# Kernel optimization log

Hardware: AMD Instinct MI355X
Metric: run time of the kernel (lower is better)

The kernel has to match this reference:

```python
import jax, jax.numpy as jnp
import numpy as np

B, T, C, L = 256, 256, 1024, 32
NEG = -1e30   # log-domain 'zero'
EPS = 1e-7    # keras.backend.epsilon()


def setup_inputs() -> dict:
    key = jax.random.key(0)
    k1, k2 = jax.random.split(key)
    # ctc_batch_cost expects softmax probabilities
    y_pred = jax.nn.softmax(jax.random.normal(k1, (B, T, C), dtype=jnp.float32), axis=-1)
    # labels in [1, C-2]: 0 is padding (count_nonzero), C-1 is the CTC blank
    y_true = jax.random.randint(k2, (B, L), 1, C - 1).astype(jnp.int32)
    return {"y_true": y_true, "y_pred": y_pred}


def _ctc_batch_cost(y_true, y_pred):
    b, t, c = y_pred.shape
    blank = c - 1                                   # TF ctc_loss: blank = last class
    lp = jnp.log(y_pred + EPS)                      # [B,T,C]
    l = y_true.shape[1]
    s = 2 * l + 1                                   # extended label length
    labels = y_true.astype(jnp.int32)
    # extended label seq: blank, l1, blank, l2, ..., blank
    ext = jnp.full((b, s), blank, jnp.int32).at[:, 1::2].set(labels)  # [B,S]
    label_len = jnp.sum((y_true != 0).astype(jnp.int32), axis=1)      # [B]
    # gather per-step log-probs of extended labels -> [B,T,S]
    lp_ext = jnp.take_along_axis(lp, jnp.broadcast_to(ext[:, None, :], (b, t, s)), axis=2)
    # skip transition s-2 -> s allowed iff ext[s] != blank and ext[s] != ext[s-2]
    prev2 = jnp.concatenate([jnp.full((b, 2), -1, jnp.int32), ext[:, :-2]], axis=1)
    allow_skip = (ext != blank) & (ext != prev2)    # [B,S]

    alpha = jnp.full((b, s), NEG, lp.dtype)
    alpha = alpha.at[:, 0].set(lp_ext[:, 0, 0]).at[:, 1].set(lp_ext[:, 0, 1])
    lp_t = jnp.transpose(lp_ext, (1, 0, 2))         # [T,B,S]

    def step(a, lpt):
        a1 = a
        a2 = jnp.concatenate([jnp.full((b, 1), NEG, a.dtype), a[:, :-1]], axis=1)
        a3 = jnp.concatenate([jnp.full((b, 2), NEG, a.dtype), a[:, :-2]], axis=1)
        a3 = jnp.where(allow_skip, a3, NEG)
        a_new = lpt + jnp.logaddexp(jnp.logaddexp(a1, a2), a3)
        return a_new, None

    alpha, _ = jax.lax.scan(step, alpha, lp_t[1:])  # input_length == T (full)
    bi = jnp.arange(b)
    idx_last_blank = 2 * label_len                  # position 2*Lb (last blank)
    idx_last_label = 2 * label_len - 1
    loss = -jnp.logaddexp(alpha[bi, idx_last_blank], alpha[bi, idx_last_label])
    return loss[:, None]                            # [B,1], matches ctc_batch_cost


def reference(y_true, y_pred):
    return _ctc_batch_cost(y_true, y_pred)
```

## Files before the change

kernel.cpp:

```cpp
#include <hip/hip_runtime.h>
#include <math.h>


#define Bt 256
#define Tt 256
#define Ct 1024
#define Lt 32
#define NEGV (-1e30f)
#define EPSV (1e-7f)
#define WAVES 16
#define TPW (Tt / WAVES)
#define STRIDE 33

__device__ __forceinline__ float lae2(float a, float b) {
    float m = fmaxf(a, b);
    return m + __logf(__expf(a - m) + __expf(b - m));
}
__device__ __forceinline__ float lae3(float a, float b, float c) {
    float m = fmaxf(fmaxf(a, b), c);
    return m + __logf(__expf(a - m) + __expf(b - m) + __expf(c - m));
}

__global__ __launch_bounds__(1024) void ctc_kernel(const int* __restrict__ y_true,
                                                   const float* __restrict__ y_pred,
                                                   float* __restrict__ out) {
    __shared__ float s_lp[Tt * STRIDE];
    __shared__ float s_alpha[66];

    const int b = blockIdx.x;
    const int tid = threadIdx.x;
    const int w = tid >> 6;
    const int lane = tid & 63;
    const int blank = Ct - 1;
    const float* yp = y_pred + (size_t)b * Tt * Ct;
    const int* lab = y_true + b * Lt;

    int cls = blank;
    if (lane < 32) cls = lab[lane];

    if (lane < 33) {
        const int t0 = w * TPW;
        float v[TPW];
        #pragma unroll
        for (int k = 0; k < TPW; ++k)
            v[k] = yp[(size_t)(t0 + k) * Ct + cls];
        #pragma unroll
        for (int k = 0; k < TPW; ++k)
            s_lp[(t0 + k) * STRIDE + lane] = __logf(v[k] + EPSV);
    }
    __syncthreads();

    if (w == 0) {
        bool allow = true;
        if (lane >= 1 && lane < 32) {
            int lprev = lab[lane - 1];
            allow = (cls != blank) && (cls != lprev);
        }

        unsigned long long nz = __ballot(lane < 32 && cls != 0);
        int ll = (int)__popcll(nz);

        float a_even, a_odd;
        {
            float le = s_lp[32];
            float lo = (lane < 32) ? s_lp[lane] : NEGV;
            a_even = (lane == 0) ? le : NEGV;
            a_odd  = (lane == 0) ? lo : NEGV;
        }

        #pragma unroll 4
        for (int t = 1; t < Tt; ++t) {
            float le = s_lp[t * STRIDE + 32];
            float lo = (lane < 32) ? s_lp[t * STRIDE + lane] : NEGV;
            float po = __shfl_up(a_odd, 1);
            if (lane == 0) po = NEGV;
            float ne = le + lae2(a_even, po);
            float no = lo + lae3(a_odd, a_even, allow ? po : NEGV);
            a_even = ne;
            a_odd  = no;
        }

        if (lane < 33) {
            s_alpha[2 * lane] = a_even;
            if (lane < 32) s_alpha[2 * lane + 1] = a_odd;
        }
        __builtin_amdgcn_s_waitcnt(0);
        if (lane == 0) {
            int i1 = 2 * ll;
            int i2 = 2 * ll - 1;
            float v1 = s_alpha[i1];
            float v2 = (i2 >= 0) ? s_alpha[i2] : NEGV;
            out[b] = -lae2(v1, v2);
        }
    }
}

extern "C" void kernel_launch(void* const* d_in, const int* in_sizes, int n_in,
                              void* d_out, int out_size, void* d_ws, size_t ws_size,
                              hipStream_t stream) {
    const int* y_true = (const int*)d_in[0];
    const float* y_pred = (const float*)d_in[1];
    float* out = (float*)d_out;
    (void)in_sizes; (void)n_in; (void)out_size; (void)d_ws; (void)ws_size;
    ctc_kernel<<<Bt, 1024, 0, stream>>>(y_true, y_pred, out);
}
```

Measured before the change: 375.4 us.

## Stream full rows via coalesced float4 loads into LDS staging before gather

Replaces scattered per-lane gathers of 33 label probabilities per time step with fully coalesced float4 reads of whole 8-row chunks of y_pred into a shared staging buffer, double-buffered through registers, then gathers from LDS. The aim is to avoid uncoalesced, latency-bound global accesses. In exchange the kernel reads the entire 1 MB per batch row instead of only the needed elements, which is about 30x more global traffic, and it adds 64 block-wide barriers.

```diff
diff --git a/kernel.cpp b/kernel.cpp
--- a/kernel.cpp
+++ b/kernel.cpp
@@ -8,9 +8,10 @@
 #define Lt 32
 #define NEGV (-1e30f)
 #define EPSV (1e-7f)
-#define WAVES 16
-#define TPW (Tt / WAVES)
-#define STRIDE 33
+#define SLP 34
+#define RPC 8
+#define NC (Tt / RPC)
+#define F4PC (RPC * Ct / 4)
 
 __device__ __forceinline__ float lae2(float a, float b) {
     float m = fmaxf(a, b);
@@ -24,7 +25,8 @@
 __global__ __launch_bounds__(1024) void ctc_kernel(const int* __restrict__ y_true,
                                                    const float* __restrict__ y_pred,
                                                    float* __restrict__ out) {
-    __shared__ float s_lp[Tt * STRIDE];
+    __shared__ float s_lp[Tt * SLP];
+    __shared__ float s_stage[RPC * Ct];
     __shared__ float s_alpha[66];
 
     const int b = blockIdx.x;
@@ -32,23 +34,40 @@
     const int w = tid >> 6;
     const int lane = tid & 63;
     const int blank = Ct - 1;
-    const float* yp = y_pred + (size_t)b * Tt * Ct;
+    const float4* yp4 = (const float4*)(y_pred + (size_t)b * Tt * Ct);
     const int* lab = y_true + b * Lt;
 
     int cls = blank;
     if (lane < 32) cls = lab[lane];
 
-    if (lane < 33) {
-        const int t0 = w * TPW;
-        float v[TPW];
-        #pragma unroll
-        for (int k = 0; k < TPW; ++k)
-            v[k] = yp[(size_t)(t0 + k) * Ct + cls];
-        #pragma unroll
-        for (int k = 0; k < TPW; ++k)
-            s_lp[(t0 + k) * STRIDE + lane] = __logf(v[k] + EPSV);
+    float4* s_stage4 = (float4*)s_stage;
+
+    {
+        float4 r0 = yp4[tid];
+        float4 r1 = yp4[tid + 1024];
+        s_stage4[tid] = r0;
+        s_stage4[tid + 1024] = r1;
     }
     __syncthreads();
+
+    for (int c = 0; c < NC; ++c) {
+        float4 r0, r1;
+        const bool more = (c + 1 < NC);
+        if (more) {
+            r0 = yp4[(c + 1) * F4PC + tid];
+            r1 = yp4[(c + 1) * F4PC + tid + 1024];
+        }
+        if (w < RPC && lane < 33) {
+            int t = c * RPC + w;
+            s_lp[t * SLP + lane] = __logf(s_stage[w * Ct + cls] + EPSV);
+        }
+        __syncthreads();
+        if (more) {
+            s_stage4[tid] = r0;
+            s_stage4[tid + 1024] = r1;
+            __syncthreads();
+        }
+    }
 
     if (w == 0) {
         bool allow = true;
@@ -56,7 +75,6 @@
             int lprev = lab[lane - 1];
             allow = (cls != blank) && (cls != lprev);
         }
-
         unsigned long long nz = __ballot(lane < 32 && cls != 0);
         int ll = (int)__popcll(nz);
 
@@ -70,8 +88,8 @@
 
         #pragma unroll 4
         for (int t = 1; t < Tt; ++t) {
-            float le = s_lp[t * STRIDE + 32];
-            float lo = (lane < 32) ? s_lp[t * STRIDE + lane] : NEGV;
+            float le = s_lp[t * SLP + 32];
+            float lo = (lane < 32) ? s_lp[t * SLP + lane] : NEGV;
             float po = __shfl_up(a_odd, 1);
             if (lane == 0) po = NEGV;
             float ne = le + lae2(a_even, po);
```

Measured after the change: 393.1 us. 4.7% more time.

## Split CTC into parallel gather kernel and single-wave recurrence kernel

Applied to the files above, without the earlier changes.

The fused per-batch kernel, with 1024 threads and a large shared buffer, is replaced by two kernels. A fully parallel gather kernel writes the log-probs of the extended labels to a workspace. A 64-thread-per-batch recurrence kernel then streams those values from global memory with a 16-deep register prefetch and uses shuffles in place of shared memory for the blank value and the final readout. The aim is to stop 15 idle waves and a large LDS allocation from limiting occupancy during the serial recurrence, and to overlap the loads with computation. In exchange it adds a workspace round trip and a second launch. The prefetch also reads past the end of each batch's rows, into the next batch's region and beyond the workspace for the last batch.

```diff
diff --git a/kernel.cpp b/kernel.cpp
--- a/kernel.cpp
+++ b/kernel.cpp
@@ -6,11 +6,10 @@
 #define Tt 256
 #define Ct 1024
 #define Lt 32
+#define NSEL 33
+#define TOTE (Bt * Tt * NSEL)
 #define NEGV (-1e30f)
 #define EPSV (1e-7f)
-#define WAVES 16
-#define TPW (Tt / WAVES)
-#define STRIDE 33
 
 __device__ __forceinline__ float lae2(float a, float b) {
     float m = fmaxf(a, b);
@@ -21,78 +20,66 @@
     return m + __logf(__expf(a - m) + __expf(b - m) + __expf(c - m));
 }
 
-__global__ __launch_bounds__(1024) void ctc_kernel(const int* __restrict__ y_true,
-                                                   const float* __restrict__ y_pred,
-                                                   float* __restrict__ out) {
-    __shared__ float s_lp[Tt * STRIDE];
-    __shared__ float s_alpha[66];
+__global__ __launch_bounds__(256) void ctc_gather(const int* __restrict__ y_true,
+                                                  const float* __restrict__ y_pred,
+                                                  float* __restrict__ ws) {
+    unsigned e = blockIdx.x * 256u + threadIdx.x;
+    unsigned row = e / 33u;
+    unsigned j = e - row * 33u;
+    unsigned b = row >> 8;
+    int cls = Ct - 1;
+    if (j < 32u) cls = y_true[(b << 5) + j];
+    float v = y_pred[((size_t)row << 10) + (unsigned)cls];
+    ws[e] = __logf(v + EPSV);
+}
 
+__global__ __launch_bounds__(64) void ctc_rec(const int* __restrict__ y_true,
+                                              const float* __restrict__ ws,
+                                              float* __restrict__ out) {
     const int b = blockIdx.x;
-    const int tid = threadIdx.x;
-    const int w = tid >> 6;
-    const int lane = tid & 63;
-    const int blank = Ct - 1;
-    const float* yp = y_pred + (size_t)b * Tt * Ct;
+    const int lane = threadIdx.x;
+    const int li = (lane < 33) ? lane : 32;
+    const float* lp = ws + (size_t)b * Tt * NSEL;
     const int* lab = y_true + b * Lt;
 
-    int cls = blank;
-    if (lane < 32) cls = lab[lane];
+    int cls = (lane < 32) ? lab[lane] : (Ct - 1);
+    bool allow = true;
+    if (lane >= 1 && lane < 32) {
+        int lprev = lab[lane - 1];
+        allow = (cls != Ct - 1) && (cls != lprev);
+    }
+    unsigned long long nz = __ballot(lane < 32 && cls != 0);
+    int ll = (int)__popcll(nz);
 
-    if (lane < 33) {
-        const int t0 = w * TPW;
-        float v[TPW];
+    float buf[16];
+    #pragma unroll
+    for (int k = 0; k < 16; ++k) buf[k] = lp[k * NSEL + li];
+
+    float a_even = NEGV, a_odd = NEGV;
+    for (int g = 0; g < 16; ++g) {
         #pragma unroll
-        for (int k = 0; k < TPW; ++k)
-            v[k] = yp[(size_t)(t0 + k) * Ct + cls];
-        #pragma unroll
-        for (int k = 0; k < TPW; ++k)
-            s_lp[(t0 + k) * STRIDE + lane] = __logf(v[k] + EPSV);
-    }
-    __syncthreads();
-
-    if (w == 0) {
-        bool allow = true;
-        if (lane >= 1 && lane < 32) {
-            int lprev = lab[lane - 1];
-            allow = (cls != blank) && (cls != lprev);
-        }
-
-        unsigned long long nz = __ballot(lane < 32 && cls != 0);
-        int ll = (int)__popcll(nz);
-
-        float a_even, a_odd;
-        {
-            float le = s_lp[32];
-            float lo = (lane < 32) ? s_lp[lane] : NEGV;
-            a_even = (lane == 0) ? le : NEGV;
-            a_odd  = (lane == 0) ? lo : NEGV;
-        }
-
-        #pragma unroll 4
-        for (int t = 1; t < Tt; ++t) {
-            float le = s_lp[t * STRIDE + 32];
-            float lo = (lane < 32) ? s_lp[t * STRIDE + lane] : NEGV;
-            float po = __shfl_up(a_odd, 1);
-            if (lane == 0) po = NEGV;
-            float ne = le + lae2(a_even, po);
-            float no = lo + lae3(a_odd, a_even, allow ? po : NEGV);
-            a_even = ne;
-            a_odd  = no;
-        }
-
-        if (lane < 33) {
-            s_alpha[2 * lane] = a_even;
-            if (lane < 32) s_alpha[2 * lane + 1] = a_odd;
-        }
-        __builtin_amdgcn_s_waitcnt(0);
-        if (lane == 0) {
-            int i1 = 2 * ll;
-            int i2 = 2 * ll - 1;
-            float v1 = s_alpha[i1];
-            float v2 = (i2 >= 0) ? s_alpha[i2] : NEGV;
-            out[b] = -lae2(v1, v2);
+        for (int k = 0; k < 16; ++k) {
+            float cur = buf[k];
+            buf[k] = lp[((unsigned)((g + 1) * 16 + k)) * NSEL + li];
+            float le = __shfl(cur, 32);
+            float lo = (lane < 32) ? cur : NEGV;
+            if (k == 0 && g == 0) {
+                a_even = (lane == 0) ? le : NEGV;
+                a_odd  = (lane == 0) ? lo : NEGV;
+            } else {
+                float po = __shfl_up(a_odd, 1);
+                if (lane == 0) po = NEGV;
+                float ne = le + lae2(a_even, po);
+                float no = lo + lae3(a_odd, a_even, allow ? po : NEGV);
+                a_even = ne;
+                a_odd  = no;
+            }
         }
     }
+
+    float v1 = __shfl(a_even, ll);
+    float v2 = (ll >= 1) ? __shfl(a_odd, ll - 1) : NEGV;
+    if (lane == 0) out[b] = -lae2(v1, v2);
 }
 
 extern "C" void kernel_launch(void* const* d_in, const int* in_sizes, int n_in,
@@ -101,6 +88,8 @@
     const int* y_true = (const int*)d_in[0];
     const float* y_pred = (const float*)d_in[1];
     float* out = (float*)d_out;
-    (void)in_sizes; (void)n_in; (void)out_size; (void)d_ws; (void)ws_size;
-    ctc_kernel<<<Bt, 1024, 0, stream>>>(y_true, y_pred, out);
+    float* ws = (float*)d_ws;
+    (void)in_sizes; (void)n_in; (void)out_size; (void)ws_size;
+    ctc_gather<<<TOTE / 256, 256, 0, stream>>>(y_true, y_pred, ws);
+    ctc_rec<<<Bt, 64, 0, stream>>>(y_true, ws, out);
 }
```

After: 373.2 us. About the same (-0.6%).
